# Performance work log

Hardware: AMD Instinct MI355X
Metric: run time of the kernel (lower is better)

The kernel has to match this reference:

```python
import jax, jax.numpy as jnp
import numpy as np

N = 50000      # nodes
E = 800000     # edges
IN = 128       # in_channels
HID = 32       # hidden_channels per head
HEADS = 4
OUT = 16       # out_channels
NEG_SLOPE_ATT = 0.2   # GATv2Conv default negative_slope
NEG_SLOPE_ACT = 0.01  # F.leaky_relu default
EPS = 1e-16


def setup_inputs() -> dict:
    key = jax.random.key(0)
    ks = jax.random.split(key, 13)
    d1 = HEADS * HID  # 128
    g = lambda k, shape, fan: jax.random.normal(k, shape, jnp.float32) * (1.0 / np.sqrt(fan))
    return {
        "x": jax.random.normal(ks[0], (N, IN), jnp.float32),
        "edge_index": jax.random.randint(ks[1], (2, E), 0, N, dtype=jnp.int32),
        "edge_weight": jax.random.uniform(ks[2], (E,), jnp.float32),
        # conv1 (GATv2): lin_l, lin_r, att, bias
        "Wl1": g(ks[3], (IN, d1), IN), "Wr1": g(ks[4], (IN, d1), IN),
        "att1": g(ks[5], (HEADS, HID), HID), "b1": jnp.zeros((d1,), jnp.float32),
        # conv2
        "Wl2": g(ks[6], (d1, d1), d1), "Wr2": g(ks[7], (d1, d1), d1),
        "att2": g(ks[8], (HEADS, HID), HID), "b2": jnp.zeros((d1,), jnp.float32),
        # classifier
        "Wc": g(ks[9], (d1, OUT), d1), "bc": jnp.zeros((OUT,), jnp.float32),
    }


def gatv2_layer(x, Wl, Wr, att, bias, src, dst):
    n = x.shape[0]
    xl = (x @ Wl).reshape(n, HEADS, HID)  # source transform
    xr = (x @ Wr).reshape(n, HEADS, HID)  # target transform
    m = xl[src] + xr[dst]                                    # [Etot, H, C]
    e = jnp.sum(jax.nn.leaky_relu(m, NEG_SLOPE_ATT) * att, axis=-1)  # [Etot, H]
    # segment softmax over incoming edges of each target node
    emax = jax.ops.segment_max(e, dst, num_segments=n)       # [N, H]
    ex = jnp.exp(e - emax[dst])
    denom = jax.ops.segment_sum(ex, dst, num_segments=n)     # [N, H]
    alpha = ex / (denom[dst] + EPS)                          # [Etot, H]
    out = jax.ops.segment_sum(xl[src] * alpha[:, :, None], dst, num_segments=n)  # [N, H, C]
    return out.reshape(n, HEADS * HID) + bias


def reference(x, edge_index, edge_weight, Wl1, Wr1, att1, b1, Wl2, Wr2, att2, b2, Wc, bc):
    # GATv2Conv default add_self_loops=True
    loops = jnp.arange(N, dtype=edge_index.dtype)
    src = jnp.concatenate([edge_index[0], loops])
    dst = jnp.concatenate([edge_index[1], loops])
    h = gatv2_layer(x, Wl1, Wr1, att1, b1, src, dst)
    h = jax.nn.leaky_relu(h, NEG_SLOPE_ACT)
    h = gatv2_layer(h, Wl2, Wr2, att2, b2, src, dst)
    h = jax.nn.leaky_relu(h, NEG_SLOPE_ACT)
    logits = h @ Wc + bc
    return (logits, h)
```

## Files before the change

kernel.cpp:

```cpp
#include <hip/hip_runtime.h>
#include <hip/hip_fp16.h>


#define LOG2E 1.4426950408889634f
#define AST 40

typedef short bf16x8 __attribute__((ext_vector_type(8)));
typedef float f32x4 __attribute__((ext_vector_type(4)));

__device__ __forceinline__ unsigned short f2bf(float f) {
  union { float f; unsigned u; } x; x.f = f;
  unsigned r = x.u + 0x7fffu + ((x.u >> 16) & 1u);
  return (unsigned short)(r >> 16);
}
__device__ __forceinline__ float bf2f(unsigned short h) {
  union { unsigned u; float f; } x; x.u = ((unsigned)h) << 16;
  return x.f;
}
__device__ __forceinline__ void split4(float4 v, ushort4& h, ushort4& l) {
  h.x = f2bf(v.x); l.x = f2bf(v.x - bf2f(h.x));
  h.y = f2bf(v.y); l.y = f2bf(v.y - bf2f(h.y));
  h.z = f2bf(v.z); l.z = f2bf(v.z - bf2f(h.z));
  h.w = f2bf(v.w); l.w = f2bf(v.w - bf2f(h.w));
}


__global__ __launch_bounds__(256) void zero_i32(int* __restrict__ p, int n) {
  int i = blockIdx.x * 256 + threadIdx.x;
  if (i < n) p[i] = 0;
}

__global__ __launch_bounds__(256) void count_kernel(const int* __restrict__ dst,
                                                    int* __restrict__ cnt,
                                                    int E, int sliceSize) {
  int slice = blockIdx.x & 7;
  int chunk = blockIdx.x >> 3;
  int nchunk = gridDim.x >> 3;
  int lo = slice * sliceSize, hi = lo + sliceSize;
  int per = (E + nchunk - 1) / nchunk;
  int b = chunk * per;
  int e = min(b + per, E);
  for (int i = b + threadIdx.x; i < e; i += 256) {
    int d = dst[i];
    if (d >= lo && d < hi) atomicAdd(&cnt[d], 1);
  }
}

__global__ __launch_bounds__(256) void scan_blk(const int* __restrict__ cnt,
                                                int* __restrict__ excl,
                                                int* __restrict__ bsum, int n) {
  __shared__ int s[256];
  int t = threadIdx.x, i = blockIdx.x * 256 + t;
  int v = (i < n) ? (cnt[i] + 1) : 0;
  s[t] = v;
  __syncthreads();
#pragma unroll
  for (int off = 1; off < 256; off <<= 1) {
    int u = (t >= off) ? s[t - off] : 0;
    __syncthreads();
    s[t] += u;
    __syncthreads();
  }
  if (i < n) excl[i] = s[t] - v;
  if (t == 255) bsum[blockIdx.x] = s[255];
}

__global__ __launch_bounds__(256) void scan_bsum(int* __restrict__ bsum, int nb,
                                                 int* __restrict__ row_start, int n) {
  __shared__ int s[256];
  int t = threadIdx.x;
  int v = (t < nb) ? bsum[t] : 0;
  s[t] = v;
  __syncthreads();
#pragma unroll
  for (int off = 1; off < 256; off <<= 1) {
    int u = (t >= off) ? s[t - off] : 0;
    __syncthreads();
    s[t] += u;
    __syncthreads();
  }
  if (t < nb) bsum[t] = s[t] - v;
  if (t == 255) row_start[n] = s[255];
}

__global__ __launch_bounds__(256) void scan_add(int* __restrict__ row_start,
                                                const int* __restrict__ bsum,
                                                int* __restrict__ wpos,
                                                int* __restrict__ csr,
                                                int n, int padBase) {
  int i = blockIdx.x * 256 + threadIdx.x;
  if (i < n) {
    int r = row_start[i] + bsum[blockIdx.x];
    row_start[i] = r;
    wpos[i] = r + 1;
    csr[r] = i;
  }
  if (blockIdx.x == 0 && threadIdx.x < 16) csr[padBase + threadIdx.x] = 0;
}

__global__ __launch_bounds__(256) void scatter_kernel(const int* __restrict__ src,
                                                      const int* __restrict__ dst,
                                                      int* __restrict__ wpos,
                                                      int* __restrict__ csr,
                                                      int E, int sliceSize) {
  int slice = blockIdx.x & 7;
  int chunk = blockIdx.x >> 3;
  int nchunk = gridDim.x >> 3;
  int lo = slice * sliceSize, hi = lo + sliceSize;
  int per = (E + nchunk - 1) / nchunk;
  int b = chunk * per;
  int e = min(b + per, E);
  for (int i = b + threadIdx.x; i < e; i += 256) {
    int d = dst[i];
    if (d >= lo && d < hi) {
      int p = atomicAdd(&wpos[d], 1);
      csr[p] = src[i];
    }
  }
}

__global__ __launch_bounds__(256) void convert_W(const float* __restrict__ Wl1,
                                                 const float* __restrict__ Wr1,
                                                 const float* __restrict__ Wl2,
                                                 const float* __restrict__ Wr2,
                                                 unsigned short* __restrict__ BT1h,
                                                 unsigned short* __restrict__ BT1l,
                                                 unsigned short* __restrict__ BT2h,
                                                 unsigned short* __restrict__ BT2l) {
  int b = blockIdx.x;
  const float* Wl = (b < 128) ? Wl1 : Wl2;
  const float* Wr = (b < 128) ? Wr1 : Wr2;
  unsigned short* BTh = (b < 128) ? BT1h : BT2h;
  unsigned short* BTl = (b < 128) ? BT1l : BT2l;
  int idx = (b & 127) * 256 + threadIdx.x;
  int col = idx >> 7, k = idx & 127;
  float v = (col < 128) ? Wl[k * 128 + col] : Wr[k * 128 + (col - 128)];
  unsigned short h = f2bf(v);
  BTh[idx] = h;
  BTl[idx] = f2bf(v - bf2f(h));
}

template <bool FP32IN>
__global__ __launch_bounds__(256) void gemm_mfma(
    const float* __restrict__ Af,
    const unsigned short* __restrict__ Ah, const unsigned short* __restrict__ Al,
    const unsigned short* __restrict__ BTh, const unsigned short* __restrict__ BTl,
    __half* __restrict__ Cl, __half* __restrict__ Cr, int nrows) {
  __shared__ unsigned short sAh[128 * AST], sAl[128 * AST];
  __shared__ unsigned short sBh[64 * AST], sBl[64 * AST];
  int tid = threadIdx.x;
  int wave = tid >> 6, lane = tid & 63;
  int rowBase = blockIdx.x * 128;
  int colBase = blockIdx.y * 64;
  int rowHalf = (wave >> 1) * 64;
  int colHalf = (wave & 1) * 32;
  int l15 = lane & 15, quad = lane >> 4;

  f32x4 acc[4][2];
#pragma unroll
  for (int m = 0; m < 4; ++m)
#pragma unroll
    for (int n = 0; n < 2; ++n) acc[m][n] = (f32x4){0.f, 0.f, 0.f, 0.f};

  for (int kc = 0; kc < 4; ++kc) {
#pragma unroll
    for (int i = 0; i < 2; ++i) {
      int idx = tid + i * 256;
      int row = idx >> 2, seg = idx & 3;
      int gr = rowBase + row;
      if (FP32IN) {
        float4 v0 = make_float4(0.f, 0.f, 0.f, 0.f), v1 = v0;
        if (gr < nrows) {
          v0 = *(const float4*)&Af[(size_t)gr * 128 + kc * 32 + seg * 8];
          v1 = *(const float4*)&Af[(size_t)gr * 128 + kc * 32 + seg * 8 + 4];
        }
        ushort4 h0, l0, h1, l1;
        split4(v0, h0, l0);
        split4(v1, h1, l1);
        *(ushort4*)&sAh[row * AST + seg * 8] = h0;
        *(ushort4*)&sAh[row * AST + seg * 8 + 4] = h1;
        *(ushort4*)&sAl[row * AST + seg * 8] = l0;
        *(ushort4*)&sAl[row * AST + seg * 8 + 4] = l1;
      } else {
        uint4 vh = make_uint4(0, 0, 0, 0), vl = make_uint4(0, 0, 0, 0);
        if (gr < nrows) {
          vh = *(const uint4*)&Ah[(size_t)gr * 128 + kc * 32 + seg * 8];
          vl = *(const uint4*)&Al[(size_t)gr * 128 + kc * 32 + seg * 8];
        }
        *(uint4*)&sAh[row * AST + seg * 8] = vh;
        *(uint4*)&sAl[row * AST + seg * 8] = vl;
      }
    }
    {
      int col = tid >> 2, seg = tid & 3;
      *(uint4*)&sBh[col * AST + seg * 8] =
          *(const uint4*)&BTh[(size_t)(colBase + col) * 128 + kc * 32 + seg * 8];
      *(uint4*)&sBl[col * AST + seg * 8] =
          *(const uint4*)&BTl[(size_t)(colBase + col) * 128 + kc * 32 + seg * 8];
    }
    __syncthreads();

    bf16x8 afh[4], afl[4], bfh[2], bfl[2];
#pragma unroll
    for (int m = 0; m < 4; ++m) {
      int r = rowHalf + m * 16 + l15;
      afh[m] = *(const bf16x8*)&sAh[r * AST + quad * 8];
      afl[m] = *(const bf16x8*)&sAl[r * AST + quad * 8];
    }
#pragma unroll
    for (int n = 0; n < 2; ++n) {
      int cc = colHalf + n * 16 + l15;
      bfh[n] = *(const bf16x8*)&sBh[cc * AST + quad * 8];
      bfl[n] = *(const bf16x8*)&sBl[cc * AST + quad * 8];
    }
#pragma unroll
    for (int m = 0; m < 4; ++m)
#pragma unroll
      for (int n = 0; n < 2; ++n) {
        acc[m][n] = __builtin_amdgcn_mfma_f32_16x16x32_bf16(afh[m], bfh[n], acc[m][n], 0, 0, 0);
        acc[m][n] = __builtin_amdgcn_mfma_f32_16x16x32_bf16(afh[m], bfl[n], acc[m][n], 0, 0, 0);
        acc[m][n] = __builtin_amdgcn_mfma_f32_16x16x32_bf16(afl[m], bfh[n], acc[m][n], 0, 0, 0);
      }
    __syncthreads();
  }

  bool isL = (colBase < 128);
  __half* __restrict__ C = isL ? Cl : Cr;
  int cb = (isL ? colBase : colBase - 128) + colHalf;
#pragma unroll
  for (int m = 0; m < 4; ++m)
#pragma unroll
    for (int r = 0; r < 4; ++r) {
      int grow = rowBase + rowHalf + m * 16 + quad * 4 + r;
      if (grow < nrows) {
#pragma unroll
        for (int n = 0; n < 2; ++n)
          C[(size_t)grow * 128 + cb + n * 16 + l15] = __float2half(acc[m][n][r]);
      }
    }
}

__global__ __launch_bounds__(256) void gat_attn(const __half* __restrict__ xl,
                                                const __half* __restrict__ xr,
                                                const int* __restrict__ row_start,
                                                const int* __restrict__ csr,
                                                const float* __restrict__ att,
                                                const float* __restrict__ bias,
                                                float* __restrict__ ofp,
                                                unsigned short* __restrict__ oh_hi,
                                                unsigned short* __restrict__ oh_lo,
                                                int n_nodes) {
  int node = blockIdx.x * 4 + (threadIdx.x >> 6);
  if (node >= n_nodes) return;
  int lane = threadIdx.x & 63;
  int slot = lane >> 4;
  int l15 = lane & 15;
  int c0 = l15 * 8;

  float fxr[8];
  {
    uint4 raw = *(const uint4*)&xr[(size_t)node * 128 + c0];
    const __half* hp = (const __half*)&raw;
#pragma unroll
    for (int k = 0; k < 8; ++k) fxr[k] = __half2float(hp[k]);
  }
  float a06[8], a04[8];
  {
    float4 a0 = *(const float4*)&att[c0];
    float4 a1 = *(const float4*)&att[c0 + 4];
    float av[8] = {a0.x, a0.y, a0.z, a0.w, a1.x, a1.y, a1.z, a1.w};
    const float C06 = 0.6f * LOG2E, C04 = 0.4f * LOG2E;
#pragma unroll
    for (int k = 0; k < 8; ++k) { a06[k] = av[k] * C06; a04[k] = av[k] * C04; }
  }

  float acc[8];
#pragma unroll
  for (int k = 0; k < 8; ++k) acc[k] = 0.f;
  float lsum = 0.f;

#define EDGE_BODY(SRC, PVALID)                                                 \
  {                                                                            \
    uint4 raw = *(const uint4*)&xl[(size_t)(unsigned)(SRC)*128 + c0];          \
    const __half* hp = (const __half*)&raw;                                    \
    float e = 0.f;                                                             \
    _Pragma("unroll") for (int k = 0; k < 8; ++k) {                            \
      float t = __half2float(hp[k]) + fxr[k];                                  \
      e = fmaf(a06[k], t, e);                                                  \
      e = fmaf(a04[k], fabsf(t), e);                                           \
    }                                                                          \
    e += __shfl_xor(e, 1);                                                     \
    e += __shfl_xor(e, 2);                                                     \
    float p = (PVALID) ? __builtin_amdgcn_exp2f(e) : 0.f;                      \
    lsum += p;                                                                 \
    _Pragma("unroll") for (int k = 0; k < 8; ++k)                              \
        acc[k] = fmaf(p, __half2float(hp[k]), acc[k]);                         \
  }

  int beg = row_start[node], end = row_start[node + 1];
  int deg = end - beg;
  int fullEnd = beg + (deg & ~15);

  for (int base = beg; base < fullEnd; base += 16) {
    int b0 = base + 4 * slot;
    int s0 = csr[b0], s1 = csr[b0 + 1], s2 = csr[b0 + 2], s3 = csr[b0 + 3];
    EDGE_BODY(s0, true);
    EDGE_BODY(s1, true);
    EDGE_BODY(s2, true);
    EDGE_BODY(s3, true);
  }
  for (int base = fullEnd; base < end; base += 4) {
    int idx = base + slot;
    int src = csr[idx];
    EDGE_BODY(src, idx < end);
  }
#undef EDGE_BODY

  lsum += __shfl_xor(lsum, 16);
  lsum += __shfl_xor(lsum, 32);
#pragma unroll
  for (int k = 0; k < 8; ++k) {
    acc[k] += __shfl_xor(acc[k], 16);
    acc[k] += __shfl_xor(acc[k], 32);
  }

  if (slot == 0) {
    float4 b0v = *(const float4*)&bias[c0];
    float4 b1v = *(const float4*)&bias[c0 + 4];
    float bv[8] = {b0v.x, b0v.y, b0v.z, b0v.w, b1v.x, b1v.y, b1v.z, b1v.w};
    float inv = 1.f / (lsum + 1e-16f);
    float o[8];
#pragma unroll
    for (int k = 0; k < 8; ++k) {
      float v = fmaf(acc[k], inv, bv[k]);
      o[k] = fmaf(0.495f, fabsf(v), 0.505f * v);
    }
    if (ofp) {
      *(float4*)&ofp[(size_t)node * 128 + c0] = make_float4(o[0], o[1], o[2], o[3]);
      *(float4*)&ofp[(size_t)node * 128 + c0 + 4] = make_float4(o[4], o[5], o[6], o[7]);
    }
    if (oh_hi) {
      ushort4 h0, l0, h1, l1;
      split4(make_float4(o[0], o[1], o[2], o[3]), h0, l0);
      split4(make_float4(o[4], o[5], o[6], o[7]), h1, l1);
      *(ushort4*)&oh_hi[(size_t)node * 128 + c0] = h0;
      *(ushort4*)&oh_hi[(size_t)node * 128 + c0 + 4] = h1;
      *(ushort4*)&oh_lo[(size_t)node * 128 + c0] = l0;
      *(ushort4*)&oh_lo[(size_t)node * 128 + c0 + 4] = l1;
    }
  }
}

__global__ __launch_bounds__(256) void classifier_kernel(const float4* __restrict__ h4,
                                                         const float* __restrict__ Wc,
                                                         const float* __restrict__ bc,
                                                         float* __restrict__ logits,
                                                         int n) {
  __shared__ float sW[2048];
  __shared__ float sb[16];
  int t = threadIdx.x;
#pragma unroll
  for (int i = 0; i < 8; ++i) sW[t + i * 256] = Wc[t + i * 256];
  if (t < 16) sb[t] = bc[t];
  __syncthreads();
  int node = blockIdx.x * 256 + t;
  if (node >= n) return;
  float acc[16];
#pragma unroll
  for (int o = 0; o < 16; ++o) acc[o] = sb[o];
  for (int c4 = 0; c4 < 32; ++c4) {
    float4 hv = h4[(unsigned)node * 32 + c4];
    const float* w = &sW[c4 * 64];
#pragma unroll
    for (int o = 0; o < 16; ++o) {
      acc[o] = fmaf(hv.x, w[o], acc[o]);
      acc[o] = fmaf(hv.y, w[16 + o], acc[o]);
      acc[o] = fmaf(hv.z, w[32 + o], acc[o]);
      acc[o] = fmaf(hv.w, w[48 + o], acc[o]);
    }
  }
#pragma unroll
  for (int q = 0; q < 4; ++q)
    *(float4*)&logits[(size_t)node * 16 + q * 4] =
        make_float4(acc[q * 4], acc[q * 4 + 1], acc[q * 4 + 2], acc[q * 4 + 3]);
}


extern "C" void kernel_launch(void* const* d_in, const int* in_sizes, int n_in,
                              void* d_out, int out_size, void* d_ws, size_t ws_size,
                              hipStream_t stream) {
  const float* x    = (const float*)d_in[0];
  const int*   ei   = (const int*)d_in[1];
  const float* Wl1  = (const float*)d_in[3];
  const float* Wr1  = (const float*)d_in[4];
  const float* att1 = (const float*)d_in[5];
  const float* b1   = (const float*)d_in[6];
  const float* Wl2  = (const float*)d_in[7];
  const float* Wr2  = (const float*)d_in[8];
  const float* att2 = (const float*)d_in[9];
  const float* b2   = (const float*)d_in[10];
  const float* Wc   = (const float*)d_in[11];
  const float* bc   = (const float*)d_in[12];

  const int N = in_sizes[0] / 128;
  const int E = in_sizes[1] / 2;

  float* outp   = (float*)d_out;
  float* logits = outp;
  float* hout   = outp + (size_t)N * 16;
  unsigned short* regionA = (unsigned short*)hout;
  unsigned short* regionB = regionA + (size_t)N * 128;

  char* ws = (char*)d_ws;
  __half* xlbuf = (__half*)ws;                ws += (size_t)N * 128 * 2;
  __half* xrbuf = (__half*)ws;                ws += (size_t)N * 128 * 2;
  unsigned short* WT1h = (unsigned short*)ws; ws += 256 * 128 * 2;
  unsigned short* WT1l = (unsigned short*)ws; ws += 256 * 128 * 2;
  unsigned short* WT2h = (unsigned short*)ws; ws += 256 * 128 * 2;
  unsigned short* WT2l = (unsigned short*)ws; ws += 256 * 128 * 2;
  int* cnt       = (int*)ws;                  ws += (size_t)N * 4;
  int* row_start = (int*)ws;                  ws += (size_t)(N + 1) * 4;
  int* wpos      = (int*)ws;                  ws += (size_t)N * 4;
  int* bsum      = (int*)ws;                  ws += 256 * 4;
  int* csr       = (int*)ws;                  ws += (size_t)(E + N + 16) * 4;

  const int* esrc = ei;
  const int* edst = ei + E;

  int gN = (N + 255) / 256;
  dim3 gGemm((N + 127) / 128, 4);
  int gAttn = (N + 3) / 4;
  int sliceSize = (N + 7) / 8;

  zero_i32<<<gN, 256, 0, stream>>>(cnt, N);
  count_kernel<<<1024, 256, 0, stream>>>(edst, cnt, E, sliceSize);
  scan_blk<<<gN, 256, 0, stream>>>(cnt, row_start, bsum, N);
  scan_bsum<<<1, 256, 0, stream>>>(bsum, gN, row_start, N);
  scan_add<<<gN, 256, 0, stream>>>(row_start, bsum, wpos, csr, N, E + N);
  scatter_kernel<<<1024, 256, 0, stream>>>(esrc, edst, wpos, csr, E, sliceSize);

  convert_W<<<256, 256, 0, stream>>>(Wl1, Wr1, Wl2, Wr2, WT1h, WT1l, WT2h, WT2l);

  gemm_mfma<true><<<gGemm, 256, 0, stream>>>(x, nullptr, nullptr, WT1h, WT1l,
                                             xlbuf, xrbuf, N);
  gat_attn<<<gAttn, 256, 0, stream>>>(xlbuf, xrbuf, row_start, csr, att1, b1,
                                      nullptr, regionA, regionB, N);

  gemm_mfma<false><<<gGemm, 256, 0, stream>>>(nullptr, regionA, regionB, WT2h, WT2l,
                                              xlbuf, xrbuf, N);
  gat_attn<<<gAttn, 256, 0, stream>>>(xlbuf, xrbuf, row_start, csr, att2, b2,
                                      hout, nullptr, nullptr, N);

  classifier_kernel<<<(N + 255) / 256, 256, 0, stream>>>((const float4*)hout, Wc, bc,
                                                         logits, N);
}
```

Measured before the change: 336.9 us.

## Store layer-1 output as fp16, widen GEMM tile, simplify edge count

```diff
diff --git a/kernel.cpp b/kernel.cpp
--- a/kernel.cpp
+++ b/kernel.cpp
@@ -31,19 +31,9 @@
 }
 
 __global__ __launch_bounds__(256) void count_kernel(const int* __restrict__ dst,
-                                                    int* __restrict__ cnt,
-                                                    int E, int sliceSize) {
-  int slice = blockIdx.x & 7;
-  int chunk = blockIdx.x >> 3;
-  int nchunk = gridDim.x >> 3;
-  int lo = slice * sliceSize, hi = lo + sliceSize;
-  int per = (E + nchunk - 1) / nchunk;
-  int b = chunk * per;
-  int e = min(b + per, E);
-  for (int i = b + threadIdx.x; i < e; i += 256) {
-    int d = dst[i];
-    if (d >= lo && d < hi) atomicAdd(&cnt[d], 1);
-  }
+                                                    int* __restrict__ cnt, int E) {
+  int i = blockIdx.x * 256 + threadIdx.x;
+  if (i < E) atomicAdd(&cnt[dst[i]], 1);
 }
 
 __global__ __launch_bounds__(256) void scan_blk(const int* __restrict__ cnt,
@@ -140,27 +130,27 @@
   BTl[idx] = f2bf(v - bf2f(h));
 }
 
-template <bool FP32IN>
+enum { IN_F32 = 0, IN_F16 = 1 };
+template <int MODE>
 __global__ __launch_bounds__(256) void gemm_mfma(
-    const float* __restrict__ Af,
-    const unsigned short* __restrict__ Ah, const unsigned short* __restrict__ Al,
+    const float* __restrict__ Af, const __half* __restrict__ Af16,
     const unsigned short* __restrict__ BTh, const unsigned short* __restrict__ BTl,
     __half* __restrict__ Cl, __half* __restrict__ Cr, int nrows) {
   __shared__ unsigned short sAh[128 * AST], sAl[128 * AST];
-  __shared__ unsigned short sBh[64 * AST], sBl[64 * AST];
+  __shared__ unsigned short sBh[128 * AST], sBl[128 * AST];
   int tid = threadIdx.x;
   int wave = tid >> 6, lane = tid & 63;
   int rowBase = blockIdx.x * 128;
-  int colBase = blockIdx.y * 64;
+  int colBase = blockIdx.y * 128;
   int rowHalf = (wave >> 1) * 64;
-  int colHalf = (wave & 1) * 32;
+  int colHalf = (wave & 1) * 64;
   int l15 = lane & 15, quad = lane >> 4;
 
-  f32x4 acc[4][2];
+  f32x4 acc[4][4];
 #pragma unroll
   for (int m = 0; m < 4; ++m)
 #pragma unroll
-    for (int n = 0; n < 2; ++n) acc[m][n] = (f32x4){0.f, 0.f, 0.f, 0.f};
+    for (int n = 0; n < 4; ++n) acc[m][n] = (f32x4){0.f, 0.f, 0.f, 0.f};
 
   for (int kc = 0; kc < 4; ++kc) {
 #pragma unroll
@@ -168,7 +158,7 @@
       int idx = tid + i * 256;
       int row = idx >> 2, seg = idx & 3;
       int gr = rowBase + row;
-      if (FP32IN) {
+      if (MODE == IN_F32) {
         float4 v0 = make_float4(0.f, 0.f, 0.f, 0.f), v1 = v0;
         if (gr < nrows) {
           v0 = *(const float4*)&Af[(size_t)gr * 128 + kc * 32 + seg * 8];
@@ -182,17 +172,27 @@
         *(ushort4*)&sAl[row * AST + seg * 8] = l0;
         *(ushort4*)&sAl[row * AST + seg * 8 + 4] = l1;
       } else {
-        uint4 vh = make_uint4(0, 0, 0, 0), vl = make_uint4(0, 0, 0, 0);
-        if (gr < nrows) {
-          vh = *(const uint4*)&Ah[(size_t)gr * 128 + kc * 32 + seg * 8];
-          vl = *(const uint4*)&Al[(size_t)gr * 128 + kc * 32 + seg * 8];
-        }
-        *(uint4*)&sAh[row * AST + seg * 8] = vh;
-        *(uint4*)&sAl[row * AST + seg * 8] = vl;
+        uint4 raw = make_uint4(0, 0, 0, 0);
+        if (gr < nrows)
+          raw = *(const uint4*)&Af16[(size_t)gr * 128 + kc * 32 + seg * 8];
+        const __half* hp = (const __half*)&raw;
+        float4 v0 = make_float4(__half2float(hp[0]), __half2float(hp[1]),
+                                __half2float(hp[2]), __half2float(hp[3]));
+        float4 v1 = make_float4(__half2float(hp[4]), __half2float(hp[5]),
+                                __half2float(hp[6]), __half2float(hp[7]));
+        ushort4 h0, l0, h1, l1;
+        split4(v0, h0, l0);
+        split4(v1, h1, l1);
+        *(ushort4*)&sAh[row * AST + seg * 8] = h0;
+        *(ushort4*)&sAh[row * AST + seg * 8 + 4] = h1;
+        *(ushort4*)&sAl[row * AST + seg * 8] = l0;
+        *(ushort4*)&sAl[row * AST + seg * 8 + 4] = l1;
       }
     }
-    {
-      int col = tid >> 2, seg = tid & 3;
+#pragma unroll
+    for (int i = 0; i < 2; ++i) {
+      int idx = tid + i * 256;
+      int col = idx >> 2, seg = idx & 3;
       *(uint4*)&sBh[col * AST + seg * 8] =
           *(const uint4*)&BTh[(size_t)(colBase + col) * 128 + kc * 32 + seg * 8];
       *(uint4*)&sBl[col * AST + seg * 8] =
@@ -200,7 +200,7 @@
     }
     __syncthreads();
 
-    bf16x8 afh[4], afl[4], bfh[2], bfl[2];
+    bf16x8 afh[4], afl[4], bfh[4], bfl[4];
 #pragma unroll
     for (int m = 0; m < 4; ++m) {
       int r = rowHalf + m * 16 + l15;
@@ -208,7 +208,7 @@
       afl[m] = *(const bf16x8*)&sAl[r * AST + quad * 8];
     }
 #pragma unroll
-    for (int n = 0; n < 2; ++n) {
+    for (int n = 0; n < 4; ++n) {
       int cc = colHalf + n * 16 + l15;
       bfh[n] = *(const bf16x8*)&sBh[cc * AST + quad * 8];
       bfl[n] = *(const bf16x8*)&sBl[cc * AST + quad * 8];
@@ -216,7 +216,7 @@
 #pragma unroll
     for (int m = 0; m < 4; ++m)
 #pragma unroll
-      for (int n = 0; n < 2; ++n) {
+      for (int n = 0; n < 4; ++n) {
         acc[m][n] = __builtin_amdgcn_mfma_f32_16x16x32_bf16(afh[m], bfh[n], acc[m][n], 0, 0, 0);
         acc[m][n] = __builtin_amdgcn_mfma_f32_16x16x32_bf16(afh[m], bfl[n], acc[m][n], 0, 0, 0);
         acc[m][n] = __builtin_amdgcn_mfma_f32_16x16x32_bf16(afl[m], bfh[n], acc[m][n], 0, 0, 0);
@@ -224,9 +224,7 @@
     __syncthreads();
   }
 
-  bool isL = (colBase < 128);
-  __half* __restrict__ C = isL ? Cl : Cr;
-  int cb = (isL ? colBase : colBase - 128) + colHalf;
+  __half* __restrict__ C = (blockIdx.y == 0) ? Cl : Cr;
 #pragma unroll
   for (int m = 0; m < 4; ++m)
 #pragma unroll
@@ -234,8 +232,8 @@
       int grow = rowBase + rowHalf + m * 16 + quad * 4 + r;
       if (grow < nrows) {
 #pragma unroll
-        for (int n = 0; n < 2; ++n)
-          C[(size_t)grow * 128 + cb + n * 16 + l15] = __float2half(acc[m][n][r]);
+        for (int n = 0; n < 4; ++n)
+          C[(size_t)grow * 128 + colHalf + n * 16 + l15] = __float2half(acc[m][n][r]);
       }
     }
 }
@@ -247,8 +245,7 @@
                                                 const float* __restrict__ att,
                                                 const float* __restrict__ bias,
                                                 float* __restrict__ ofp,
-                                                unsigned short* __restrict__ oh_hi,
-                                                unsigned short* __restrict__ oh_lo,
+                                                __half* __restrict__ oh16,
                                                 int n_nodes) {
   int node = blockIdx.x * 4 + (threadIdx.x >> 6);
   if (node >= n_nodes) return;
@@ -339,14 +336,18 @@
       *(float4*)&ofp[(size_t)node * 128 + c0] = make_float4(o[0], o[1], o[2], o[3]);
       *(float4*)&ofp[(size_t)node * 128 + c0 + 4] = make_float4(o[4], o[5], o[6], o[7]);
     }
-    if (oh_hi) {
-      ushort4 h0, l0, h1, l1;
-      split4(make_float4(o[0], o[1], o[2], o[3]), h0, l0);
-      split4(make_float4(o[4], o[5], o[6], o[7]), h1, l1);
-      *(ushort4*)&oh_hi[(size_t)node * 128 + c0] = h0;
-      *(ushort4*)&oh_hi[(size_t)node * 128 + c0 + 4] = h1;
-      *(ushort4*)&oh_lo[(size_t)node * 128 + c0] = l0;
-      *(ushort4*)&oh_lo[(size_t)node * 128 + c0 + 4] = l1;
+    if (oh16) {
+      ushort4 ha, hb;
+      ha.x = __half_as_ushort(__float2half(o[0]));
+      ha.y = __half_as_ushort(__float2half(o[1]));
+      ha.z = __half_as_ushort(__float2half(o[2]));
+      ha.w = __half_as_ushort(__float2half(o[3]));
+      hb.x = __half_as_ushort(__float2half(o[4]));
+      hb.y = __half_as_ushort(__float2half(o[5]));
+      hb.z = __half_as_ushort(__float2half(o[6]));
+      hb.w = __half_as_ushort(__float2half(o[7]));
+      *(ushort4*)&oh16[(size_t)node * 128 + c0] = ha;
+      *(ushort4*)&oh16[(size_t)node * 128 + c0 + 4] = hb;
     }
   }
 }
@@ -408,8 +409,7 @@
   float* outp   = (float*)d_out;
   float* logits = outp;
   float* hout   = outp + (size_t)N * 16;
-  unsigned short* regionA = (unsigned short*)hout;
-  unsigned short* regionB = regionA + (size_t)N * 128;
+  __half* h1f16 = (__half*)hout;
 
   char* ws = (char*)d_ws;
   __half* xlbuf = (__half*)ws;                ws += (size_t)N * 128 * 2;
@@ -427,13 +427,13 @@
   const int* esrc = ei;
   const int* edst = ei + E;
 
-  int gN = (N + 255) / 256;
-  dim3 gGemm((N + 127) / 128, 4);
+  int gN = (N + 255) / 256, gE = (E + 255) / 256;
+  dim3 gGemm((N + 127) / 128, 2);
   int gAttn = (N + 3) / 4;
   int sliceSize = (N + 7) / 8;
 
   zero_i32<<<gN, 256, 0, stream>>>(cnt, N);
-  count_kernel<<<1024, 256, 0, stream>>>(edst, cnt, E, sliceSize);
+  count_kernel<<<gE, 256, 0, stream>>>(edst, cnt, E);
   scan_blk<<<gN, 256, 0, stream>>>(cnt, row_start, bsum, N);
   scan_bsum<<<1, 256, 0, stream>>>(bsum, gN, row_start, N);
   scan_add<<<gN, 256, 0, stream>>>(row_start, bsum, wpos, csr, N, E + N);
@@ -441,15 +441,15 @@
 
   convert_W<<<256, 256, 0, stream>>>(Wl1, Wr1, Wl2, Wr2, WT1h, WT1l, WT2h, WT2l);
 
-  gemm_mfma<true><<<gGemm, 256, 0, stream>>>(x, nullptr, nullptr, WT1h, WT1l,
-                                             xlbuf, xrbuf, N);
+  gemm_mfma<IN_F32><<<gGemm, 256, 0, stream>>>(x, nullptr, WT1h, WT1l,
+                                               xlbuf, xrbuf, N);
   gat_attn<<<gAttn, 256, 0, stream>>>(xlbuf, xrbuf, row_start, csr, att1, b1,
-                                      nullptr, regionA, regionB, N);
-
-  gemm_mfma<false><<<gGemm, 256, 0, stream>>>(nullptr, regionA, regionB, WT2h, WT2l,
-                                              xlbuf, xrbuf, N);
+                                      nullptr, h1f16, N);
+
+  gemm_mfma<IN_F16><<<gGemm, 256, 0, stream>>>(nullptr, h1f16, WT2h, WT2l,
+                                               xlbuf, xrbuf, N);
   gat_attn<<<gAttn, 256, 0, stream>>>(xlbuf, xrbuf, row_start, csr, att2, b2,
-                                      hout, nullptr, nullptr, N);
+                                      hout, nullptr, N);
 
   classifier_kernel<<<(N + 255) / 256, 256, 0, stream>>>((const float4*)hout, Wc, bc,
                                                          logits, N);
```

Measured after the change: 325.7 us. 3.3% less time.
